# Performance work log

Measured on AMD Instinct MI355X. Metric: run time of the kernel, lower is better.

## Reference

```python
import jax, jax.numpy as jnp
import numpy as np

# Module config (matches init_kwargs)
SHAPE = (32, 32)          # wire grid
KERNEL = (3, 3)           # window per dim
NUM_LAYERS = 4
NINPUTS = int(np.prod(KERNEL))        # 9
NPOS = 2 ** NINPUTS                   # 512 possible boolean input combos


def _bitmask():
    # itertools.product(range(2), repeat=NINPUTS) then transpose -> (NINPUTS, NPOS)
    # combination j, window-element m has bit (j >> (NINPUTS-1-m)) & 1
    j = jnp.arange(NPOS)
    m = jnp.arange(NINPUTS)
    return ((j[None, :] >> (NINPUTS - 1 - m)[:, None]) & 1).astype(jnp.float32)


def _convolve(x):
    # x: (B, H, W) -> (B, H, W, K) wrapped sliding windows (im2col via rolls),
    # faithful to ASIC.convolve with kernel_offset='center'.
    out = x
    for d, k in enumerate(KERNEL):
        # window element i along dim d comes from position +i (wraparound)
        out = jnp.stack([jnp.roll(out, -i, axis=1 + d) for i in range(k)], axis=out.ndim)
    out = out.reshape(x.shape + (-1,))  # (B, H, W, K) with k0 slowest-varying
    # 'center' offset: roll by prod((k-1)//2) along the LAST spatial dim (as the torch code does)
    shift = int(np.prod([(k - 1) // 2 for k in KERNEL]))
    out = jnp.roll(out, shift, axis=len(KERNEL))  # axis = last spatial axis in (B, H, W, K)
    return out


def setup_inputs() -> dict:
    key = jax.random.key(0)
    k1, k2 = jax.random.split(key)
    x = jax.random.uniform(k1, (16,) + SHAPE, dtype=jnp.float32)
    toggle_gates = jax.random.uniform(k2, (NUM_LAYERS, NPOS) + SHAPE, dtype=jnp.float32)
    return {"x": x, "toggle_gates": toggle_gates}


def reference(x, toggle_gates):
    tw = jax.nn.sigmoid(toggle_gates)       # (L, NPOS, H, W)
    bits = _bitmask()                        # (NINPUTS, NPOS)
    # embed(): shape == x spatial shape -> stride-1 slices; initial state is x, output is full state
    state = x                                # (B, H, W)
    for layer in range(NUM_LAYERS):
        conv = _convolve(state)              # (B, H, W, K)
        # soft-LUT weights: prod over window elems of (1 - |bit - input|)
        w = jnp.prod(1.0 - jnp.abs(conv[..., None] - bits), axis=-2)  # (B, H, W, NPOS)
        state = jnp.clip(jnp.einsum('bhwp,phw->bhw', w, tw[layer]), 0.0, 1.0)
    return state
```

## Files before the change

kernel.cpp:

```cpp
#include <hip/hip_runtime.h>

#define HH 32
#define WW 32
#define NPOS 512
#define TILE 8
#define PPAD 516
#define NTHR 512
#define NBLK 128
#define NLAYERS 4
#define RPAD 33

__device__ __forceinline__ float ld_dev(const float* p) {
    return __hip_atomic_load(p, __ATOMIC_RELAXED, __HIP_MEMORY_SCOPE_AGENT);
}
__device__ __forceinline__ void st_dev(float* p, float v) {
    __hip_atomic_store(p, v, __ATOMIC_RELAXED, __HIP_MEMORY_SCOPE_AGENT);
}

__device__ __forceinline__ void grid_barrier(int* cnt) {
    __syncthreads();
    if (threadIdx.x == 0) {
        __hip_atomic_fetch_add(cnt, 1, __ATOMIC_RELAXED, __HIP_MEMORY_SCOPE_AGENT);
        while (__hip_atomic_load(cnt, __ATOMIC_RELAXED, __HIP_MEMORY_SCOPE_AGENT) < NBLK) {
            __builtin_amdgcn_s_sleep(8);
        }
    }
    __syncthreads();
}

__device__ __forceinline__ void make_v(const float c[9], float* v) {
    float a2[2], a4[4], a8[8], a16[16];
    a2[0] = 1.0f - c[4]; a2[1] = c[4];
    #pragma unroll
    for (int i = 0; i < 2; ++i)  { a4[2*i]  = a2[i]  * (1.0f - c[5]); a4[2*i+1]  = a2[i]  * c[5]; }
    #pragma unroll
    for (int i = 0; i < 4; ++i)  { a8[2*i]  = a4[i]  * (1.0f - c[6]); a8[2*i+1]  = a4[i]  * c[6]; }
    #pragma unroll
    for (int i = 0; i < 8; ++i)  { a16[2*i] = a8[i]  * (1.0f - c[7]); a16[2*i+1] = a8[i]  * c[7]; }
    #pragma unroll
    for (int i = 0; i < 16; ++i) { v[2*i]   = a16[i] * (1.0f - c[8]); v[2*i+1]   = a16[i] * c[8]; }
}

__global__ __launch_bounds__(NTHR) void asic_fused(
    const float* __restrict__ x,
    const float* __restrict__ tg,
    float* __restrict__ bufA,
    float* __restrict__ bufB,
    float* __restrict__ out,
    int* __restrict__ bar)
{
    __shared__ float  lut[NLAYERS][TILE * PPAD];
    __shared__ float2 red[2][8 * RPAD];

    const int t     = threadIdx.x;
    const int hw0   = blockIdx.x * TILE;
    const int h     = hw0 >> 5;
    const int w0    = hw0 & 31;

    #pragma unroll
    for (int k = 0; k < 32; ++k) {
        int f     = t + NTHR * k;
        int layer = f >> 12;
        int r     = f & 4095;
        int p     = r >> 3;
        int pos   = r & 7;
        float g = tg[(size_t)layer * NPOS * HH * WW + p * (HH * WW) + hw0 + pos];
        lut[layer][pos * PPAD + p] = __builtin_amdgcn_rcpf(1.0f + __expf(-g));
    }

    const int th    = t & 255;
    const int bhalf = t >> 8;
    const int hwl   = th & 7;
    const int bp    = (th >> 3) & 3;
    const int oct   = th >> 5;
    const int w     = w0 + hwl;
    const int b0    = bhalf * 8 + 2 * bp;

    const int bit0 = (oct >> 2) & 1, bit1 = (oct >> 1) & 1, bit2 = oct & 1;

    const float* src = x;

    for (int layer = 0; layer < NLAYERS; ++layer) {
        float* dst = (layer == 3) ? out : ((layer & 1) ? bufB : bufA);

        float c0[9], c1[9];
        const float* s0 = src + b0 * (HH * WW);
        const float* s1 = s0 + (HH * WW);
        #pragma unroll
        for (int i = 0; i < 3; ++i) {
            int row = ((h + i) & 31) * 32;
            #pragma unroll
            for (int j = 0; j < 3; ++j) {
                int idx = row + ((w + j - 1 + 32) & 31);
                c0[3 * i + j] = ld_dev(s0 + idx);
                c1[3 * i + j] = ld_dev(s1 + idx);
            }
        }

        if (layer == 0) __syncthreads();

        float v0[32], v1[32];
        make_v(c0, v0);
        make_v(c1, v1);

        float base0 = (bit0 ? c0[0] : 1.0f - c0[0]) * (bit1 ? c0[1] : 1.0f - c0[1]) * (bit2 ? c0[2] : 1.0f - c0[2]);
        float base1 = (bit0 ? c1[0] : 1.0f - c1[0]) * (bit1 ? c1[1] : 1.0f - c1[1]) * (bit2 ? c1[2] : 1.0f - c1[2]);
        float uA0 = base0 * (1.0f - c0[3]), uB0 = base0 * c0[3];
        float uA1 = base1 * (1.0f - c1[3]), uB1 = base1 * c1[3];

        const float4* lutp = (const float4*)(&lut[layer][0] + hwl * PPAD);
        const float4* A = lutp + (2 * oct) * 8;
        const float4* B = A + 8;
        float sA0 = 0.f, sA1 = 0.f, sB0 = 0.f, sB1 = 0.f;
        #pragma unroll
        for (int l4 = 0; l4 < 8; ++l4) {
            float4 LA = A[l4];
            float4 LB = B[l4];
            sA0 = fmaf(LA.x, v0[4*l4+0], sA0); sA0 = fmaf(LA.y, v0[4*l4+1], sA0);
            sA0 = fmaf(LA.z, v0[4*l4+2], sA0); sA0 = fmaf(LA.w, v0[4*l4+3], sA0);
            sA1 = fmaf(LA.x, v1[4*l4+0], sA1); sA1 = fmaf(LA.y, v1[4*l4+1], sA1);
            sA1 = fmaf(LA.z, v1[4*l4+2], sA1); sA1 = fmaf(LA.w, v1[4*l4+3], sA1);
            sB0 = fmaf(LB.x, v0[4*l4+0], sB0); sB0 = fmaf(LB.y, v0[4*l4+1], sB0);
            sB0 = fmaf(LB.z, v0[4*l4+2], sB0); sB0 = fmaf(LB.w, v0[4*l4+3], sB0);
            sB1 = fmaf(LB.x, v1[4*l4+0], sB1); sB1 = fmaf(LB.y, v1[4*l4+1], sB1);
            sB1 = fmaf(LB.z, v1[4*l4+2], sB1); sB1 = fmaf(LB.w, v1[4*l4+3], sB1);
        }
        float acc0 = fmaf(uA0, sA0, uB0 * sB0);
        float acc1 = fmaf(uA1, sA1, uB1 * sB1);

        if (layer > 0) __syncthreads();
        red[bhalf][oct * RPAD + bp * 8 + hwl] = make_float2(acc0, acc1);
        __syncthreads();

        if (th < 64) {
            int hw  = th & 7;
            int bl  = th >> 3;
            int bpi = bl >> 1, par = bl & 1;
            float s = 0.0f;
            #pragma unroll
            for (int o = 0; o < 8; ++o) {
                float2 r = red[bhalf][o * RPAD + bpi * 8 + hw];
                s += par ? r.y : r.x;
            }
            s = fminf(fmaxf(s, 0.0f), 1.0f);
            st_dev(dst + (size_t)(bhalf * 8 + bl) * (HH * WW) + h * 32 + w0 + hw, s);
        }

        if (layer < NLAYERS - 1) grid_barrier(bar + layer);
        src = dst;
    }
}

extern "C" void kernel_launch(void* const* d_in, const int* in_sizes, int n_in,
                              void* d_out, int out_size, void* d_ws, size_t ws_size,
                              hipStream_t stream) {
    const float* x  = (const float*)d_in[0];
    const float* tg = (const float*)d_in[1];
    float* out  = (float*)d_out;
    float* bufA = (float*)d_ws;
    float* bufB = bufA + 16 * HH * WW;
    int*   bar  = (int*)((char*)d_ws + 256 * 1024);

    hipMemsetAsync(bar, 0, 4 * sizeof(int), stream);
    asic_fused<<<NBLK, NTHR, 0, stream>>>(x, tg, bufA, bufB, out, bar);
}
```

Measured before the change: 81.36 us.

## Replace global grid barrier with per-tile neighbor flag synchronization

Swaps the all-block atomic counter barrier between layers for per-block ready flags, so each block waits only on the 9 tiles its 3x3 stencil reads. A third intermediate buffer is added so that a fast block cannot overwrite data a slower neighbor still reads. This targets the cost of waiting on the slowest block across the whole grid at each layer, and adds a few more flag polls and a larger memset.

```diff
diff --git a/kernel.cpp b/kernel.cpp
--- a/kernel.cpp
+++ b/kernel.cpp
@@ -9,6 +9,7 @@
 #define NBLK 128
 #define NLAYERS 4
 #define RPAD 33
+#define FSTR 16
 
 __device__ __forceinline__ float ld_dev(const float* p) {
     return __hip_atomic_load(p, __ATOMIC_RELAXED, __HIP_MEMORY_SCOPE_AGENT);
@@ -17,12 +18,19 @@
     __hip_atomic_store(p, v, __ATOMIC_RELAXED, __HIP_MEMORY_SCOPE_AGENT);
 }
 
-__device__ __forceinline__ void grid_barrier(int* cnt) {
+__device__ __forceinline__ void neighbor_sync(int* flags, int layer, int h, int seg) {
     __syncthreads();
-    if (threadIdx.x == 0) {
-        __hip_atomic_fetch_add(cnt, 1, __ATOMIC_RELAXED, __HIP_MEMORY_SCOPE_AGENT);
-        while (__hip_atomic_load(cnt, __ATOMIC_RELAXED, __HIP_MEMORY_SCOPE_AGENT) < NBLK) {
-            __builtin_amdgcn_s_sleep(8);
+    const int t = threadIdx.x;
+    if (t == 0) {
+        __hip_atomic_store(&flags[(layer * NBLK + (h * 4 + seg)) * FSTR], 1,
+                           __ATOMIC_RELAXED, __HIP_MEMORY_SCOPE_AGENT);
+    }
+    if (t < 9) {
+        int dr = t / 3, ds = t % 3 - 1;
+        int pid = (((h + dr) & 31) << 2) | ((seg + ds) & 3);
+        const int* f = &flags[(layer * NBLK + pid) * FSTR];
+        while (__hip_atomic_load(f, __ATOMIC_RELAXED, __HIP_MEMORY_SCOPE_AGENT) == 0) {
+            __builtin_amdgcn_s_sleep(2);
         }
     }
     __syncthreads();
@@ -46,16 +54,20 @@
     const float* __restrict__ tg,
     float* __restrict__ bufA,
     float* __restrict__ bufB,
+    float* __restrict__ bufC,
     float* __restrict__ out,
-    int* __restrict__ bar)
+    int* __restrict__ flags)
 {
     __shared__ float  lut[NLAYERS][TILE * PPAD];
     __shared__ float2 red[2][8 * RPAD];
 
-    const int t     = threadIdx.x;
-    const int hw0   = blockIdx.x * TILE;
-    const int h     = hw0 >> 5;
-    const int w0    = hw0 & 31;
+    const int t    = threadIdx.x;
+    const int bid  = blockIdx.x;
+    const int hrow = bid >> 2;
+    const int seg  = bid & 3;
+    const int hw0  = bid * TILE;
+    const int h    = hrow;
+    const int w0   = seg * TILE;
 
     #pragma unroll
     for (int k = 0; k < 32; ++k) {
@@ -78,10 +90,11 @@
 
     const int bit0 = (oct >> 2) & 1, bit1 = (oct >> 1) & 1, bit2 = oct & 1;
 
+    float* dsts[NLAYERS] = {bufA, bufB, bufC, out};
     const float* src = x;
 
     for (int layer = 0; layer < NLAYERS; ++layer) {
-        float* dst = (layer == 3) ? out : ((layer & 1) ? bufB : bufA);
+        float* dst = dsts[layer];
 
         float c0[9], c1[9];
         const float* s0 = src + b0 * (HH * WW);
@@ -146,7 +159,7 @@
             st_dev(dst + (size_t)(bhalf * 8 + bl) * (HH * WW) + h * 32 + w0 + hw, s);
         }
 
-        if (layer < NLAYERS - 1) grid_barrier(bar + layer);
+        if (layer < NLAYERS - 1) neighbor_sync(flags, layer, h, seg);
         src = dst;
     }
 }
@@ -159,8 +172,9 @@
     float* out  = (float*)d_out;
     float* bufA = (float*)d_ws;
     float* bufB = bufA + 16 * HH * WW;
-    int*   bar  = (int*)((char*)d_ws + 256 * 1024);
+    float* bufC = bufB + 16 * HH * WW;
+    int*   flags = (int*)((char*)d_ws + 256 * 1024);
 
-    hipMemsetAsync(bar, 0, 4 * sizeof(int), stream);
-    asic_fused<<<NBLK, NTHR, 0, stream>>>(x, tg, bufA, bufB, out, bar);
+    hipMemsetAsync(flags, 0, 3 * NBLK * FSTR * sizeof(int), stream);
+    asic_fused<<<NBLK, NTHR, 0, stream>>>(x, tg, bufA, bufB, bufC, out, flags);
 }
```

New measurement: 75.82 us. -6.8%, faster.
